# Performance work log

Hardware: AMD Instinct MI355X
Metric: run time of the kernel (lower is better)

The kernel has to match this reference:

```python
import jax, jax.numpy as jnp
import numpy as np

N_NODES = 50000
N_EDGES = 1000000
IN_C = 128
HID_C = 128
N_REL = 8


def rgcn_conv(x, W, root, b, src, dst, et, n_rel):
    # PyG-style RGCNConv: per-relation linear transform of source features,
    # mean-aggregated per (target node, relation), plus root transform + bias.
    n = x.shape[0]
    h = jnp.einsum('nd,rdh->nrh', x, W)          # [N, R, H] per-relation transforms
    msgs = h[src, et]                            # [E, H] gather per-edge message
    seg = dst * n_rel + et                       # combined (node, relation) segment id
    agg = jax.ops.segment_sum(msgs, seg, num_segments=n * n_rel)        # [N*R, H]
    cnt = jax.ops.segment_sum(jnp.ones_like(msgs[:, 0]), seg, num_segments=n * n_rel)
    agg = agg / jnp.maximum(cnt, 1.0)[:, None]   # mean over edges of each relation
    return agg.reshape(n, n_rel, -1).sum(axis=1) + x @ root + b


def setup_inputs() -> dict:
    key = jax.random.key(0)
    ks = jax.random.split(key, 12)
    s = 1.0 / np.sqrt(IN_C)
    sh = 1.0 / np.sqrt(HID_C)
    return {
        'x': jax.random.normal(ks[0], (N_NODES, IN_C), dtype=jnp.float32),
        'ei': jax.random.randint(ks[1], (2, N_EDGES), 0, N_NODES, dtype=jnp.int32),
        'et': jax.random.randint(ks[2], (N_EDGES,), 0, N_REL, dtype=jnp.int32),
        'W1': jax.random.normal(ks[3], (N_REL, IN_C, HID_C), dtype=jnp.float32) * s,
        'root1': jax.random.normal(ks[4], (IN_C, HID_C), dtype=jnp.float32) * s,
        'b1': jnp.zeros((HID_C,), dtype=jnp.float32),
        'W2': jax.random.normal(ks[5], (N_REL, HID_C, HID_C), dtype=jnp.float32) * sh,
        'root2': jax.random.normal(ks[6], (HID_C, HID_C), dtype=jnp.float32) * sh,
        'b2': jnp.zeros((HID_C,), dtype=jnp.float32),
        'lin_W': jax.random.normal(ks[7], (HID_C, HID_C), dtype=jnp.float32) * sh,
        'lin_b': jnp.zeros((HID_C,), dtype=jnp.float32),
    }


def reference(x, ei, et, W1, root1, b1, W2, root2, b2, lin_W, lin_b):
    src, dst = ei[0], ei[1]
    h = jax.nn.relu(rgcn_conv(x, W1, root1, b1, src, dst, et, N_REL))
    h = rgcn_conv(h, W2, root2, b2, src, dst, et, N_REL)
    return h @ lin_W + lin_b
```

## Files before the change

### kernel.cpp

```cpp
#include <hip/hip_runtime.h>
#include <hip/hip_bf16.h>

#define N_NODES 50000
#define N_EDGES 1000000
#define C       128
#define N_REL   8
#define N_SEG   (N_NODES * N_REL)
#define KTOT    (N_REL * C + C)
#define KC_CNT  (KTOT / 32)
#define A_STRIDE 1160
#define NCHUNK  ((N_SEG + 1023) / 1024)
#define MV_N    (N_SEG + 1 + N_EDGES)
#define NBLK    (N_NODES / 16)
#define FE_BLK  ((N_EDGES + 511) / 512)

typedef __hip_bfloat16  bf16;
typedef __hip_bfloat162 bf162;
typedef __attribute__((ext_vector_type(8))) short short8;
typedef __attribute__((ext_vector_type(4))) float f32x4;

__device__ __forceinline__ size_t frag_index(int k, int n) {
    int nt = n >> 4, n15 = n & 15;
    int kc = k >> 5, quad = (k >> 3) & 3, j = k & 7;
    int lane = quad * 16 + n15;
    return ((size_t)(nt * KC_CNT + kc) * 64 + lane) * 8 + j;
}

#define CVT_BLOCKS ((N_NODES * C / 2) / 256)
#define CNT_BLOCKS ((N_EDGES + 255) / 256)
__global__ void prep_kernel(const float2* __restrict__ xf, unsigned int* __restrict__ xb,
                            const int* __restrict__ dst, const int* __restrict__ et,
                            int* __restrict__ cnt) {
    int bid = blockIdx.x;
    if (bid < CVT_BLOCKS) {
        int i = bid * 256 + threadIdx.x;
        float2 v = xf[i];
        union { bf162 h; unsigned int u; } cv;
        cv.h = bf162(__float2bfloat16(v.x), __float2bfloat16(v.y));
        xb[i] = cv.u;
    } else {
        int e = (bid - CVT_BLOCKS) * 256 + threadIdx.x;
        if (e < N_EDGES) atomicAdd(&cnt[dst[e] * N_REL + et[e]], 1);
    }
}

#define RP_B  (KTOT * C / 256)
#define RPT_B ((KTOT / 16) * (C / 16))
__global__ void scanA_kernel(const int* __restrict__ cnt, int* __restrict__ offs,
                             int* __restrict__ partials,
                             const float* __restrict__ W1, const float* __restrict__ root1,
                             const float* __restrict__ W2, const float* __restrict__ root2,
                             const float* __restrict__ linW,
                             const float* __restrict__ b2, const float* __restrict__ linb,
                             bf16* __restrict__ Bp1, bf16* __restrict__ Bp2,
                             float* __restrict__ b2p) {
    int bid = blockIdx.x;
    int t   = threadIdx.x;
    if (bid < NCHUNK) {
        __shared__ int tot[256];
        int base = bid * 1024 + t * 4;
        int v0 = (base + 0 < N_SEG) ? cnt[base + 0] : 0;
        int v1 = (base + 1 < N_SEG) ? cnt[base + 1] : 0;
        int v2 = (base + 2 < N_SEG) ? cnt[base + 2] : 0;
        int v3 = (base + 3 < N_SEG) ? cnt[base + 3] : 0;
        int tsum = v0 + v1 + v2 + v3;
        tot[t] = tsum;
        __syncthreads();
        for (int d = 1; d < 256; d <<= 1) {
            int x = tot[t];
            int y = (t >= d) ? tot[t - d] : 0;
            __syncthreads();
            tot[t] = x + y;
            __syncthreads();
        }
        int excl = tot[t] - tsum;
        if (base + 0 < N_SEG) offs[base + 0] = excl;
        if (base + 1 < N_SEG) offs[base + 1] = excl + v0;
        if (base + 2 < N_SEG) offs[base + 2] = excl + v0 + v1;
        if (base + 3 < N_SEG) offs[base + 3] = excl + v0 + v1 + v2;
        if (t == 255) partials[bid] = tot[255];
    } else if (bid < NCHUNK + RP_B) {
        int idx = (bid - NCHUNK) * 256 + t;
        int k = idx >> 7, n = idx & 127;
        float val;
        if (k < N_REL * C) val = W1[(size_t)k * C + n];
        else               val = root1[(size_t)(k - N_REL * C) * C + n];
        Bp1[frag_index(k, n)] = __float2bfloat16(val);
    } else if (bid < NCHUNK + RP_B + RPT_B) {
        __shared__ float Wt[16][128];
        __shared__ float Lt[128][16];
        int tileid = bid - NCHUNK - RP_B;
        int kt = tileid >> 3;
        int n0 = (tileid & 7) * 16;
        int k0 = kt * 16;
        const float* baseW = (k0 < N_REL * C) ? (W2 + (size_t)k0 * C)
                                              : (root2 + (size_t)(k0 - N_REL * C) * C);
#pragma unroll
        for (int r = 0; r < 8; r++) {
            int idx = t + r * 256;
            Wt[idx >> 7][idx & 127] = baseW[idx];
        }
#pragma unroll
        for (int r = 0; r < 8; r++) {
            int idx = t + r * 256;
            Lt[idx >> 4][idx & 15] = linW[(size_t)(idx >> 4) * C + n0 + (idx & 15)];
        }
        __syncthreads();
        int ty = t >> 4, tx = t & 15;
        float acc = 0.f;
#pragma unroll 8
        for (int m = 0; m < 128; m++)
            acc += Wt[ty][m] * Lt[m][tx];
        Bp2[frag_index(k0 + ty, n0 + tx)] = __float2bfloat16(acc);
    } else {
        if (t < 128) {
            float acc = linb[t];
            for (int m = 0; m < C; m++)
                acc += b2[m] * linW[(size_t)m * C + t];
            b2p[t] = acc;
        }
    }
}

__global__ void fillB_kernel(const int* __restrict__ src, const int* __restrict__ dst,
                             const int* __restrict__ et,
                             const int* __restrict__ offs_raw,
                             const int* __restrict__ partials,
                             int* __restrict__ offs_final,
                             int* __restrict__ ticket,
                             int* __restrict__ srcs_out) {
    __shared__ int s[512];
    int t = threadIdx.x;
    int bid = blockIdx.x;
    s[t] = (t < NCHUNK) ? partials[t] : 0;
    __syncthreads();
    for (int d = 1; d < 512; d <<= 1) {
        int x = s[t];
        int y = (t >= d) ? s[t - d] : 0;
        __syncthreads();
        s[t] = x + y;
        __syncthreads();
    }
    if (bid < NCHUNK) {
        int add = (bid == 0) ? 0 : s[bid - 1];
        int base = bid * 1024 + t * 2;
#pragma unroll
        for (int j = 0; j < 2; j++) {
            int idx = base + j;
            if (idx < N_SEG) offs_final[idx] = offs_raw[idx] + add;
        }
        if (bid == 0 && t == 0) offs_final[N_SEG] = N_EDGES;
    } else {
        int e = (bid - NCHUNK) * 512 + t;
        if (e < N_EDGES) {
            int seg = dst[e] * N_REL + et[e];
            int chunk = seg >> 10;
            int base = offs_raw[seg] + ((chunk == 0) ? 0 : s[chunk - 1]);
            int pos = base + atomicAdd(&ticket[seg], 1);
            srcs_out[pos] = src[e];
        }
    }
}

template <int RELU, int OUT_F32, int COPY_CSR>
__global__ __launch_bounds__(512, 6) void fused_layer(
        const unsigned int* __restrict__ featu,
        const int*   __restrict__ offs,
        const int*   __restrict__ srcs,
        const short8* __restrict__ Bp,
        const float* __restrict__ bias,
        void* __restrict__ outp,
        int* __restrict__ offs2, int* __restrict__ srcs2)
{
    __shared__ __align__(16) unsigned int At[16 * (A_STRIDE / 2)];
    __shared__ int offsL[129];
    const int tid  = threadIdx.x;
    const int lane = tid & 63;
    const int w    = tid >> 6;
    const int v0   = blockIdx.x * 16;

    if (tid < 129) offsL[tid] = offs[v0 * 8 + tid];
    if (tid < 64)  At[(tid >> 2) * (A_STRIDE / 2) + 576 + (tid & 3)] = 0u;

    if (COPY_CSR) {
        for (int i = blockIdx.x * 512 + tid; i < MV_N; i += NBLK * 512) {
            if (i < N_SEG + 1) offs2[i] = offs[i];
            else               srcs2[i - (N_SEG + 1)] = srcs[i - (N_SEG + 1)];
        }
    }

    for (int q = tid; q < 16 * 64; q += 512) {
        int node = q >> 6, pch = q & 63;
        At[node * (A_STRIDE / 2) + 512 + pch] = featu[(size_t)(v0 + node) * 64 + pch];
    }
    __syncthreads();

    {
        const int segLo = w * 16;
        const int segHi = segLo + 16;
        int curSeg = segLo;
        int segEnd = offsL[curSeg + 1];
        int i      = offsL[segLo];
        const int eend = offsL[segHi];
        float a0 = 0.f, a1 = 0.f;

        unsigned int vals[16];
        bool have = (i + 16 <= eend);
        if (have) {
            const int ib = __builtin_amdgcn_readfirstlane(i);
            int sv[16];
#pragma unroll
            for (int j = 0; j < 16; j++) sv[j] = srcs[ib + j];
#pragma unroll
            for (int j = 0; j < 16; j++) vals[j] = featu[(size_t)sv[j] * 64 + lane];
        }
        while (have) {
            const int inext = i + 16;
            const bool havenext = (inext + 16 <= eend);
            unsigned int vals2[16];
            if (havenext) {
                const int ib2 = __builtin_amdgcn_readfirstlane(inext);
                int sv2[16];
#pragma unroll
                for (int j = 0; j < 16; j++) sv2[j] = srcs[ib2 + j];
#pragma unroll
                for (int j = 0; j < 16; j++) vals2[j] = featu[(size_t)sv2[j] * 64 + lane];
            }
#pragma unroll
            for (int j = 0; j < 16; j++) {
                while (i + j == segEnd) {
                    int b = offsL[curSeg];
                    float inv = (segEnd > b) ? 1.0f / (float)(segEnd - b) : 0.0f;
                    union { bf162 h; unsigned int u; } cv;
                    cv.h = bf162(__float2bfloat16(a0 * inv), __float2bfloat16(a1 * inv));
                    At[(curSeg >> 3) * (A_STRIDE / 2) + (curSeg & 7) * 64 + lane] = cv.u;
                    a0 = 0.f; a1 = 0.f;
                    curSeg++;
                    segEnd = offsL[curSeg + 1];
                }
                union { bf162 h; unsigned int u; } uv; uv.u = vals[j];
                a0 += __low2float(uv.h);
                a1 += __high2float(uv.h);
            }
            i = inext;
            have = havenext;
            if (havenext) {
#pragma unroll
                for (int j = 0; j < 16; j++) vals[j] = vals2[j];
            }
        }
        {
            int m = eend - i;
            const int ib = __builtin_amdgcn_readfirstlane(i);
            int sv[16];
#pragma unroll
            for (int j = 0; j < 16; j++) if (j < m) sv[j] = srcs[ib + j];
            unsigned int tvals[16];
#pragma unroll
            for (int j = 0; j < 16; j++) if (j < m) tvals[j] = featu[(size_t)sv[j] * 64 + lane];
#pragma unroll
            for (int j = 0; j < 16; j++) {
                if (j < m) {
                    while (i + j == segEnd) {
                        int b = offsL[curSeg];
                        float inv = (segEnd > b) ? 1.0f / (float)(segEnd - b) : 0.0f;
                        union { bf162 h; unsigned int u; } cv;
                        cv.h = bf162(__float2bfloat16(a0 * inv), __float2bfloat16(a1 * inv));
                        At[(curSeg >> 3) * (A_STRIDE / 2) + (curSeg & 7) * 64 + lane] = cv.u;
                        a0 = 0.f; a1 = 0.f;
                        curSeg++;
                        segEnd = offsL[curSeg + 1];
                    }
                    union { bf162 h; unsigned int u; } uv; uv.u = tvals[j];
                    a0 += __low2float(uv.h);
                    a1 += __high2float(uv.h);
                }
            }
        }
        while (curSeg < segHi) {
            int b = offsL[curSeg], e2 = offsL[curSeg + 1];
            float inv = (e2 > b) ? 1.0f / (float)(e2 - b) : 0.0f;
            union { bf162 h; unsigned int u; } cv;
            cv.h = bf162(__float2bfloat16(a0 * inv), __float2bfloat16(a1 * inv));
            At[(curSeg >> 3) * (A_STRIDE / 2) + (curSeg & 7) * 64 + lane] = cv.u;
            a0 = 0.f; a1 = 0.f;
            curSeg++;
        }
    }
    __syncthreads();

    const int quad = lane >> 4, n15 = lane & 15;
    f32x4 acc = {0.f, 0.f, 0.f, 0.f};
    const short* Ash = (const short*)At;

    short8 b0 = Bp[(size_t)(w * KC_CNT) * 64 + lane];
#pragma unroll 4
    for (int kc = 0; kc < KC_CNT; kc++) {
        short8 cb0 = b0;
        if (kc + 1 < KC_CNT)
            b0 = Bp[(size_t)(w * KC_CNT + kc + 1) * 64 + lane];
        short8 a = *reinterpret_cast<const short8*>(Ash + n15 * A_STRIDE + kc * 32 + quad * 8);
        acc = __builtin_amdgcn_mfma_f32_16x16x32_bf16(a, cb0, acc, 0, 0, 0);
    }

    {
        int col = w * 16 + n15;
        float bv = bias[col];
#pragma unroll
        for (int r = 0; r < 4; r++) {
            int m = quad * 4 + r;
            float v = acc[r] + bv;
            if (RELU) v = fmaxf(v, 0.f);
            if (OUT_F32) ((float*)outp)[(size_t)(v0 + m) * C + col] = v;
            else         ((bf16*)outp)[(size_t)(v0 + m) * C + col] = __float2bfloat16(v);
        }
    }
}

extern "C" void kernel_launch(void* const* d_in, const int* in_sizes, int n_in,
                              void* d_out, int out_size, void* d_ws, size_t ws_size,
                              hipStream_t stream) {
    const float* x     = (const float*)d_in[0];
    const int*   ei    = (const int*)d_in[1];
    const int*   et    = (const int*)d_in[2];
    const float* W1    = (const float*)d_in[3];
    const float* root1 = (const float*)d_in[4];
    const float* b1    = (const float*)d_in[5];
    const float* W2    = (const float*)d_in[6];
    const float* root2 = (const float*)d_in[7];
    const float* b2    = (const float*)d_in[8];
    const float* linW  = (const float*)d_in[9];
    const float* linb  = (const float*)d_in[10];
    const int* src = ei;
    const int* dst = ei + N_EDGES;

    char* ob = (char*)d_out;
    int* cnt_i    = (int*)(ob + 0);
    int* ticket   = (int*)(ob + 1600000);
    int* offs_t   = (int*)(ob + 3200000);
    int* partials = (int*)(ob + 4800256);
    int* offs_f   = (int*)(ob + 4803072);
    int* srcs_t   = (int*)(ob + 6403328);
    unsigned int* xb16 = (unsigned int*)(ob + 10485760);

    char* eb = (char*)d_in[1];
    int* offs2 = (int*)(eb + 0);
    int* srcs2 = (int*)(eb + 1600256);

    char* xbuf = (char*)d_in[0];
    unsigned int* h1 = (unsigned int*)xbuf;
    bf16*  Bp1 = (bf16*)(xbuf + 13000192);
    bf16*  Bp2 = (bf16*)(xbuf + 13295360);
    float* b2p = (float*)(xbuf + 13590528);

    float* out = (float*)d_out;

    hipMemsetAsync(cnt_i, 0, 3200000, stream);
    prep_kernel<<<CVT_BLOCKS + CNT_BLOCKS, 256, 0, stream>>>(
        (const float2*)x, xb16, dst, et, cnt_i);
    scanA_kernel<<<NCHUNK + RP_B + RPT_B + 1, 256, 0, stream>>>(
        cnt_i, offs_t, partials, W1, root1, W2, root2, linW, b2, linb,
        Bp1, Bp2, b2p);
    fillB_kernel<<<NCHUNK + FE_BLK, 512, 0, stream>>>(
        src, dst, et, offs_t, partials, offs_f, ticket, srcs_t);

    fused_layer<1, 0, 1><<<NBLK, 512, 0, stream>>>(
        xb16, offs_f, srcs_t, (const short8*)Bp1, b1, (void*)h1, offs2, srcs2);
    fused_layer<0, 1, 0><<<NBLK, 512, 0, stream>>>(
        h1, offs2, srcs2, (const short8*)Bp2, b2p, (void*)out, nullptr, nullptr);

    (void)in_sizes; (void)n_in; (void)out_size; (void)d_ws; (void)ws_size;
}
```

Baseline: 325.4 us.

## Record atomic rank in count pass, drop ticket atomics, and ping-pong gather buffers

The counting pass now stores each edge's atomicAdd return value as its rank within its (node, relation) segment. The fill pass then scatters sources directly to base+rank, which removes the second atomic pass and the ticket buffer and halves the memset. The gather loop in the fused layer is restructured with two ping-pong register buffers instead of copying vals2 into vals. It also keeps segment bounds in scalar registers via readfirstlane and converts bf16 to float with bit shifts and a packed float2 add. This adds a 4MB rank buffer write and read, and reshuffles the scratch layout in the output buffer.

After: 303.0 us. -6.9%, faster.

```diff
diff --git a/kernel.cpp b/kernel.cpp
--- a/kernel.cpp
+++ b/kernel.cpp
@@ -18,6 +18,7 @@
 typedef __hip_bfloat162 bf162;
 typedef __attribute__((ext_vector_type(8))) short short8;
 typedef __attribute__((ext_vector_type(4))) float f32x4;
+typedef __attribute__((ext_vector_type(2))) float f32x2;
 
 __device__ __forceinline__ size_t frag_index(int k, int n) {
     int nt = n >> 4, n15 = n & 15;
@@ -30,7 +31,7 @@
 #define CNT_BLOCKS ((N_EDGES + 255) / 256)
 __global__ void prep_kernel(const float2* __restrict__ xf, unsigned int* __restrict__ xb,
                             const int* __restrict__ dst, const int* __restrict__ et,
-                            int* __restrict__ cnt) {
+                            int* __restrict__ cnt, int* __restrict__ rank) {
     int bid = blockIdx.x;
     if (bid < CVT_BLOCKS) {
         int i = bid * 256 + threadIdx.x;
@@ -40,7 +41,7 @@
         xb[i] = cv.u;
     } else {
         int e = (bid - CVT_BLOCKS) * 256 + threadIdx.x;
-        if (e < N_EDGES) atomicAdd(&cnt[dst[e] * N_REL + et[e]], 1);
+        if (e < N_EDGES) rank[e] = atomicAdd(&cnt[dst[e] * N_REL + et[e]], 1);
     }
 }
 
@@ -127,7 +128,7 @@
                              const int* __restrict__ offs_raw,
                              const int* __restrict__ partials,
                              int* __restrict__ offs_final,
-                             int* __restrict__ ticket,
+                             const int* __restrict__ rank,
                              int* __restrict__ srcs_out) {
     __shared__ int s[512];
     int t = threadIdx.x;
@@ -156,8 +157,7 @@
             int seg = dst[e] * N_REL + et[e];
             int chunk = seg >> 10;
             int base = offs_raw[seg] + ((chunk == 0) ? 0 : s[chunk - 1]);
-            int pos = base + atomicAdd(&ticket[seg], 1);
-            srcs_out[pos] = src[e];
+            srcs_out[base + rank[e]] = src[e];
         }
     }
 }
@@ -197,94 +197,92 @@
 
     {
         const int segLo = w * 16;
-        const int segHi = segLo + 16;
         int curSeg = segLo;
-        int segEnd = offsL[curSeg + 1];
-        int i      = offsL[segLo];
-        const int eend = offsL[segHi];
-        float a0 = 0.f, a1 = 0.f;
-
-        unsigned int vals[16];
-        bool have = (i + 16 <= eend);
-        if (have) {
-            const int ib = __builtin_amdgcn_readfirstlane(i);
+        int i      = __builtin_amdgcn_readfirstlane(offsL[segLo]);
+        int segBeg = i;
+        int segEnd = __builtin_amdgcn_readfirstlane(offsL[segLo + 1]);
+        const int eend = __builtin_amdgcn_readfirstlane(offsL[segLo + 16]);
+        f32x2 acc2 = {0.f, 0.f};
+
+        auto FLUSH = [&](int upto) {
+            while (segEnd == upto) {
+                float inv = (segEnd > segBeg) ? 1.0f / (float)(segEnd - segBeg) : 0.0f;
+                union { bf162 h; unsigned int u; } cv;
+                cv.h = bf162(__float2bfloat16(acc2.x * inv), __float2bfloat16(acc2.y * inv));
+                At[(curSeg >> 3) * (A_STRIDE / 2) + (curSeg & 7) * 64 + lane] = cv.u;
+                acc2.x = 0.f; acc2.y = 0.f;
+                segBeg = segEnd;
+                curSeg++;
+                segEnd = __builtin_amdgcn_readfirstlane(offsL[curSeg + 1]);
+            }
+        };
+        auto LOADF = [&](unsigned int (&v)[16], int base) {
             int sv[16];
 #pragma unroll
-            for (int j = 0; j < 16; j++) sv[j] = srcs[ib + j];
-#pragma unroll
-            for (int j = 0; j < 16; j++) vals[j] = featu[(size_t)sv[j] * 64 + lane];
-        }
-        while (have) {
-            const int inext = i + 16;
-            const bool havenext = (inext + 16 <= eend);
-            unsigned int vals2[16];
-            if (havenext) {
-                const int ib2 = __builtin_amdgcn_readfirstlane(inext);
-                int sv2[16];
-#pragma unroll
-                for (int j = 0; j < 16; j++) sv2[j] = srcs[ib2 + j];
-#pragma unroll
-                for (int j = 0; j < 16; j++) vals2[j] = featu[(size_t)sv2[j] * 64 + lane];
+            for (int j = 0; j < 16; j++) sv[j] = srcs[base + j];
+#pragma unroll
+            for (int j = 0; j < 16; j++) v[j] = featu[(size_t)sv[j] * 64 + lane];
+        };
+        auto FOLD16 = [&](unsigned int (&v)[16]) {
+#pragma unroll
+            for (int j = 0; j < 16; j++) {
+                FLUSH(i + j);
+                union { unsigned int u; float f; } lo, hi;
+                lo.u = v[j] << 16;
+                hi.u = v[j] & 0xFFFF0000u;
+                f32x2 tadd = {lo.f, hi.f};
+                acc2 += tadd;
             }
-#pragma unroll
-            for (int j = 0; j < 16; j++) {
-                while (i + j == segEnd) {
-                    int b = offsL[curSeg];
-                    float inv = (segEnd > b) ? 1.0f / (float)(segEnd - b) : 0.0f;
-                    union { bf162 h; unsigned int u; } cv;
-                    cv.h = bf162(__float2bfloat16(a0 * inv), __float2bfloat16(a1 * inv));
-                    At[(curSeg >> 3) * (A_STRIDE / 2) + (curSeg & 7) * 64 + lane] = cv.u;
-                    a0 = 0.f; a1 = 0.f;
-                    curSeg++;
-                    segEnd = offsL[curSeg + 1];
-                }
-                union { bf162 h; unsigned int u; } uv; uv.u = vals[j];
-                a0 += __low2float(uv.h);
-                a1 += __high2float(uv.h);
+            i += 16;
+        };
+
+        unsigned int valsA[16], valsB[16];
+        const int nfull = (eend - i) >> 4;
+        if (nfull > 0) {
+            LOADF(valsA, i);
+            int b = 0;
+            while (true) {
+                if (b + 1 < nfull) LOADF(valsB, i + 16);
+                FOLD16(valsA);
+                b++;
+                if (b >= nfull) break;
+                if (b + 1 < nfull) LOADF(valsA, i + 16);
+                FOLD16(valsB);
+                b++;
+                if (b >= nfull) break;
             }
-            i = inext;
-            have = havenext;
-            if (havenext) {
-#pragma unroll
-                for (int j = 0; j < 16; j++) vals[j] = vals2[j];
-            }
         }
         {
-            int m = eend - i;
-            const int ib = __builtin_amdgcn_readfirstlane(i);
-            int sv[16];
-#pragma unroll
-            for (int j = 0; j < 16; j++) if (j < m) sv[j] = srcs[ib + j];
-            unsigned int tvals[16];
-#pragma unroll
-            for (int j = 0; j < 16; j++) if (j < m) tvals[j] = featu[(size_t)sv[j] * 64 + lane];
-#pragma unroll
-            for (int j = 0; j < 16; j++) {
-                if (j < m) {
-                    while (i + j == segEnd) {
-                        int b = offsL[curSeg];
-                        float inv = (segEnd > b) ? 1.0f / (float)(segEnd - b) : 0.0f;
-                        union { bf162 h; unsigned int u; } cv;
-                        cv.h = bf162(__float2bfloat16(a0 * inv), __float2bfloat16(a1 * inv));
-                        At[(curSeg >> 3) * (A_STRIDE / 2) + (curSeg & 7) * 64 + lane] = cv.u;
-                        a0 = 0.f; a1 = 0.f;
-                        curSeg++;
-                        segEnd = offsL[curSeg + 1];
+            const int m = eend - i;
+            if (m > 0) {
+                int sv[16];
+#pragma unroll
+                for (int j = 0; j < 16; j++) if (j < m) sv[j] = srcs[i + j];
+#pragma unroll
+                for (int j = 0; j < 16; j++) if (j < m) valsA[j] = featu[(size_t)sv[j] * 64 + lane];
+#pragma unroll
+                for (int j = 0; j < 16; j++) {
+                    if (j < m) {
+                        FLUSH(i + j);
+                        union { unsigned int u; float f; } lo, hi;
+                        lo.u = valsA[j] << 16;
+                        hi.u = valsA[j] & 0xFFFF0000u;
+                        f32x2 tadd = {lo.f, hi.f};
+                        acc2 += tadd;
                     }
-                    union { bf162 h; unsigned int u; } uv; uv.u = tvals[j];
-                    a0 += __low2float(uv.h);
-                    a1 += __high2float(uv.h);
                 }
             }
         }
-        while (curSeg < segHi) {
-            int b = offsL[curSeg], e2 = offsL[curSeg + 1];
-            float inv = (e2 > b) ? 1.0f / (float)(e2 - b) : 0.0f;
+        while (curSeg < segLo + 16) {
+            float inv = (segEnd > segBeg) ? 1.0f / (float)(segEnd - segBeg) : 0.0f;
             union { bf162 h; unsigned int u; } cv;
-            cv.h = bf162(__float2bfloat16(a0 * inv), __float2bfloat16(a1 * inv));
+            cv.h = bf162(__float2bfloat16(acc2.x * inv), __float2bfloat16(acc2.y * inv));
             At[(curSeg >> 3) * (A_STRIDE / 2) + (curSeg & 7) * 64 + lane] = cv.u;
-            a0 = 0.f; a1 = 0.f;
+            acc2.x = 0.f; acc2.y = 0.f;
+            segBeg = segEnd;
             curSeg++;
+            if (curSeg < segLo + 16)
+                segEnd = __builtin_amdgcn_readfirstlane(offsL[curSeg + 1]);
         }
     }
     __syncthreads();
@@ -336,12 +334,12 @@
 
     char* ob = (char*)d_out;
     int* cnt_i    = (int*)(ob + 0);
-    int* ticket   = (int*)(ob + 1600000);
-    int* offs_t   = (int*)(ob + 3200000);
-    int* partials = (int*)(ob + 4800256);
-    int* offs_f   = (int*)(ob + 4803072);
-    int* srcs_t   = (int*)(ob + 6403328);
-    unsigned int* xb16 = (unsigned int*)(ob + 10485760);
+    int* offs_f   = (int*)(ob + 0);
+    int* offs_t   = (int*)(ob + 1600256);
+    int* partials = (int*)(ob + 3200256);
+    int* srcs_t   = (int*)(ob + 3202048);
+    int* rank     = (int*)(ob + 7202048);
+    unsigned int* xb16 = (unsigned int*)(ob + 11202048);
 
     char* eb = (char*)d_in[1];
     int* offs2 = (int*)(eb + 0);
@@ -355,14 +353,14 @@
 
     float* out = (float*)d_out;
 
-    hipMemsetAsync(cnt_i, 0, 3200000, stream);
+    hipMemsetAsync(cnt_i, 0, 1600000, stream);
     prep_kernel<<<CVT_BLOCKS + CNT_BLOCKS, 256, 0, stream>>>(
-        (const float2*)x, xb16, dst, et, cnt_i);
+        (const float2*)x, xb16, dst, et, cnt_i, rank);
     scanA_kernel<<<NCHUNK + RP_B + RPT_B + 1, 256, 0, stream>>>(
         cnt_i, offs_t, partials, W1, root1, W2, root2, linW, b2, linb,
         Bp1, Bp2, b2p);
     fillB_kernel<<<NCHUNK + FE_BLK, 512, 0, stream>>>(
-        src, dst, et, offs_t, partials, offs_f, ticket, srcs_t);
+        src, dst, et, offs_t, partials, offs_f, rank, srcs_t);
 
     fused_layer<1, 0, 1><<<NBLK, 512, 0, stream>>>(
         xb16, offs_f, srcs_t, (const short8*)Bp1, b1, (void*)h1, offs2, srcs2);
```

## Record per-edge rank during counting and defer chunk-offset fixup into layer kernel

Applied to the files above, without the earlier changes.

The counting pass now stores each edge's atomic return value as its rank within its segment, so the CSR fill no longer needs a second ticket atomic pass. The fill kernel writes sources directly at base+rank. Finalizing the offsets is moved out of the fill kernel into the first layer kernel, which adds the per-chunk prefix (spx) on the fly. The ticket buffer and half of the memset go away, at the cost of an extra 4MB rank array write and read.

Measured after the change: 296.8 us. 8.8% less time.

```diff
diff --git a/kernel.cpp b/kernel.cpp
--- a/kernel.cpp
+++ b/kernel.cpp
@@ -30,7 +30,7 @@
 #define CNT_BLOCKS ((N_EDGES + 255) / 256)
 __global__ void prep_kernel(const float2* __restrict__ xf, unsigned int* __restrict__ xb,
                             const int* __restrict__ dst, const int* __restrict__ et,
-                            int* __restrict__ cnt) {
+                            int* __restrict__ cnt, int* __restrict__ rank) {
     int bid = blockIdx.x;
     if (bid < CVT_BLOCKS) {
         int i = bid * 256 + threadIdx.x;
@@ -40,7 +40,7 @@
         xb[i] = cv.u;
     } else {
         int e = (bid - CVT_BLOCKS) * 256 + threadIdx.x;
-        if (e < N_EDGES) atomicAdd(&cnt[dst[e] * N_REL + et[e]], 1);
+        if (e < N_EDGES) rank[e] = atomicAdd(&cnt[dst[e] * N_REL + et[e]], 1);
     }
 }
 
@@ -126,9 +126,9 @@
                              const int* __restrict__ et,
                              const int* __restrict__ offs_raw,
                              const int* __restrict__ partials,
-                             int* __restrict__ offs_final,
-                             int* __restrict__ ticket,
-                             int* __restrict__ srcs_out) {
+                             const int* __restrict__ rank,
+                             int* __restrict__ srcs_out,
+                             int* __restrict__ spx) {
     __shared__ int s[512];
     int t = threadIdx.x;
     int bid = blockIdx.x;
@@ -141,28 +141,17 @@
         s[t] = x + y;
         __syncthreads();
     }
-    if (bid < NCHUNK) {
-        int add = (bid == 0) ? 0 : s[bid - 1];
-        int base = bid * 1024 + t * 2;
-#pragma unroll
-        for (int j = 0; j < 2; j++) {
-            int idx = base + j;
-            if (idx < N_SEG) offs_final[idx] = offs_raw[idx] + add;
-        }
-        if (bid == 0 && t == 0) offs_final[N_SEG] = N_EDGES;
-    } else {
-        int e = (bid - NCHUNK) * 512 + t;
-        if (e < N_EDGES) {
-            int seg = dst[e] * N_REL + et[e];
-            int chunk = seg >> 10;
-            int base = offs_raw[seg] + ((chunk == 0) ? 0 : s[chunk - 1]);
-            int pos = base + atomicAdd(&ticket[seg], 1);
-            srcs_out[pos] = src[e];
-        }
-    }
-}
-
-template <int RELU, int OUT_F32, int COPY_CSR>
+    if (bid == 0 && t < NCHUNK) spx[t] = (t == 0) ? 0 : s[t - 1];
+    int e = bid * 512 + t;
+    if (e < N_EDGES) {
+        int seg = dst[e] * N_REL + et[e];
+        int chunk = seg >> 10;
+        int base = offs_raw[seg] + ((chunk == 0) ? 0 : s[chunk - 1]);
+        srcs_out[base + rank[e]] = src[e];
+    }
+}
+
+template <int RELU, int OUT_F32, int COPY_CSR, int RAWOFFS>
 __global__ __launch_bounds__(512, 6) void fused_layer(
         const unsigned int* __restrict__ featu,
         const int*   __restrict__ offs,
@@ -170,7 +159,8 @@
         const short8* __restrict__ Bp,
         const float* __restrict__ bias,
         void* __restrict__ outp,
-        int* __restrict__ offs2, int* __restrict__ srcs2)
+        int* __restrict__ offs2, int* __restrict__ srcs2,
+        const int* __restrict__ spx)
 {
     __shared__ __align__(16) unsigned int At[16 * (A_STRIDE / 2)];
     __shared__ int offsL[129];
@@ -179,13 +169,25 @@
     const int w    = tid >> 6;
     const int v0   = blockIdx.x * 16;
 
-    if (tid < 129) offsL[tid] = offs[v0 * 8 + tid];
+    if (tid < 129) {
+        int idx = v0 * 8 + tid;
+        int val;
+        if (RAWOFFS) val = (idx < N_SEG) ? offs[idx] + spx[idx >> 10] : N_EDGES;
+        else         val = offs[idx];
+        offsL[tid] = val;
+    }
     if (tid < 64)  At[(tid >> 2) * (A_STRIDE / 2) + 576 + (tid & 3)] = 0u;
 
     if (COPY_CSR) {
         for (int i = blockIdx.x * 512 + tid; i < MV_N; i += NBLK * 512) {
-            if (i < N_SEG + 1) offs2[i] = offs[i];
-            else               srcs2[i - (N_SEG + 1)] = srcs[i - (N_SEG + 1)];
+            if (i < N_SEG + 1) {
+                int val;
+                if (RAWOFFS) val = (i < N_SEG) ? offs[i] + spx[i >> 10] : N_EDGES;
+                else         val = offs[i];
+                offs2[i] = val;
+            } else {
+                srcs2[i - (N_SEG + 1)] = srcs[i - (N_SEG + 1)];
+            }
         }
     }
 
@@ -336,12 +338,12 @@
 
     char* ob = (char*)d_out;
     int* cnt_i    = (int*)(ob + 0);
-    int* ticket   = (int*)(ob + 1600000);
-    int* offs_t   = (int*)(ob + 3200000);
-    int* partials = (int*)(ob + 4800256);
-    int* offs_f   = (int*)(ob + 4803072);
-    int* srcs_t   = (int*)(ob + 6403328);
-    unsigned int* xb16 = (unsigned int*)(ob + 10485760);
+    int* offs_t   = (int*)(ob + 1600000);
+    int* partials = (int*)(ob + 3200000);
+    int* spx      = (int*)(ob + 3201792);
+    int* srcs_t   = (int*)(ob + 3203584);
+    int* rank     = (int*)(ob + 7203584);
+    unsigned int* xb16 = (unsigned int*)(ob + 11203584);
 
     char* eb = (char*)d_in[1];
     int* offs2 = (int*)(eb + 0);
@@ -355,19 +357,19 @@
 
     float* out = (float*)d_out;
 
-    hipMemsetAsync(cnt_i, 0, 3200000, stream);
+    hipMemsetAsync(cnt_i, 0, 1600000, stream);
     prep_kernel<<<CVT_BLOCKS + CNT_BLOCKS, 256, 0, stream>>>(
-        (const float2*)x, xb16, dst, et, cnt_i);
+        (const float2*)x, xb16, dst, et, cnt_i, rank);
     scanA_kernel<<<NCHUNK + RP_B + RPT_B + 1, 256, 0, stream>>>(
         cnt_i, offs_t, partials, W1, root1, W2, root2, linW, b2, linb,
         Bp1, Bp2, b2p);
-    fillB_kernel<<<NCHUNK + FE_BLK, 512, 0, stream>>>(
-        src, dst, et, offs_t, partials, offs_f, ticket, srcs_t);
-
-    fused_layer<1, 0, 1><<<NBLK, 512, 0, stream>>>(
-        xb16, offs_f, srcs_t, (const short8*)Bp1, b1, (void*)h1, offs2, srcs2);
-    fused_layer<0, 1, 0><<<NBLK, 512, 0, stream>>>(
-        h1, offs2, srcs2, (const short8*)Bp2, b2p, (void*)out, nullptr, nullptr);
+    fillB_kernel<<<FE_BLK, 512, 0, stream>>>(
+        src, dst, et, offs_t, partials, rank, srcs_t, spx);
+
+    fused_layer<1, 0, 1, 1><<<NBLK, 512, 0, stream>>>(
+        xb16, offs_t, srcs_t, (const short8*)Bp1, b1, (void*)h1, offs2, srcs2, spx);
+    fused_layer<0, 1, 0, 0><<<NBLK, 512, 0, stream>>>(
+        h1, offs2, srcs2, (const short8*)Bp2, b2p, (void*)out, nullptr, nullptr, nullptr);
 
     (void)in_sizes; (void)n_in; (void)out_size; (void)d_ws; (void)ws_size;
 }
```
